# Kernel tuning notes

Measured on AMD Instinct MI355X. Metric: run time of the kernel, lower is better.

## Reference

```python
import jax, jax.numpy as jnp
import numpy as np

NUM_HEADS = 16
EMBED_DIM = 1024
HEAD_DIM = EMBED_DIM // NUM_HEADS
SCALE = HEAD_DIM * -0.5  # faithful to source: multiplicative, negative


def setup_inputs() -> dict:
    key = jax.random.key(0)
    kx, kq, kk, kv, ko = jax.random.split(key, 5)
    B, S, E = 2, 2048, EMBED_DIM
    std = 1.0 / np.sqrt(E)
    return {
        "x": jax.random.normal(kx, (B, S, E), dtype=jnp.float32),
        "Wq": jax.random.normal(kq, (E, E), dtype=jnp.float32) * std,
        "Wk": jax.random.normal(kk, (E, E), dtype=jnp.float32) * std,
        "Wv": jax.random.normal(kv, (E, E), dtype=jnp.float32) * std,
        "Wo": jax.random.normal(ko, (E, E), dtype=jnp.float32) * std,
    }


def reference(x, Wq, Wk, Wv, Wo):
    B, S, E = x.shape
    H, D = NUM_HEADS, HEAD_DIM
    # nn.Linear(bias=False): y = x @ W.T
    q = (x @ Wq.T).reshape(B, S, H, D).transpose(0, 2, 1, 3)  # unused downstream (faithful to source)
    k = (x @ Wk.T).reshape(B, S, H, D).transpose(0, 2, 1, 3)  # [B,H,S,D]
    v = (x @ Wv.T).reshape(B, S, H, D).transpose(0, 2, 1, 3)
    # Source bug reproduced: logits = K @ V^T, scaled by head_dim * -0.5
    logits = jnp.einsum('bhsd,bhtd->bhst', k, v) * SCALE  # [B,H,S,S]
    attn = jax.nn.softmax(logits, axis=-1)
    out = jnp.einsum('bhst,bhtd->bhsd', attn, v)  # [B,H,S,D]
    out = out.transpose(0, 2, 1, 3).reshape(B, S, E)
    return out @ Wo.T
```

## Files before the change

kernel.cpp:

```cpp
#include <hip/hip_runtime.h>
#include <math.h>

#define B_ 2
#define S_ 2048
#define E_ 1024
#define H_ 16
#define D_ 64
#define M_ (B_ * S_)
#define SC2 (-46.166241308446828f)

typedef unsigned short u16;
typedef __attribute__((ext_vector_type(8))) short short8;
typedef __attribute__((ext_vector_type(16))) float f32x16;

static __device__ __forceinline__ u16 bf16_rne(float x) {
    unsigned u = __float_as_uint(x);
    u += 0x7FFFu + ((u >> 16) & 1u);
    return (u16)(u >> 16);
}
static __device__ __forceinline__ float bf16f(u16 h) {
    return __uint_as_float(((unsigned)h) << 16);
}
static __device__ __forceinline__ f32x16 mfma_b(short8 a, short8 b, f32x16 c) {
    return __builtin_amdgcn_mfma_f32_32x32x16_bf16(a, b, c, 0, 0, 0);
}
static __device__ __forceinline__ unsigned pack2(u16 a, u16 b) {
    return (unsigned)a | ((unsigned)b << 16);
}

__global__ __launch_bounds__(256)
void convert_split(const float* __restrict__ x, const float* __restrict__ Wk,
                   const float* __restrict__ Wv, const float* __restrict__ Wo,
                   u16* __restrict__ Xh, u16* __restrict__ Xl,
                   u16* __restrict__ Wkh, u16* __restrict__ Wkl,
                   u16* __restrict__ Wvh, u16* __restrict__ Wvl,
                   u16* __restrict__ Woh, u16* __restrict__ Wol)
{
    const int blk = blockIdx.x;
    const float* src; u16 *dh, *dl; int base;
    if (blk < 4096)      { src = x;  dh = Xh;  dl = Xl;  base = blk; }
    else if (blk < 5120) { src = Wk; dh = Wkh; dl = Wkl; base = blk - 4096; }
    else if (blk < 6144) { src = Wv; dh = Wvh; dl = Wvl; base = blk - 5120; }
    else                 { src = Wo; dh = Woh; dl = Wol; base = blk - 6144; }
    const size_t off = ((size_t)base * 256 + threadIdx.x) * 4;
    const float4 v = *(const float4*)(src + off);
    const float f[4] = {v.x, v.y, v.z, v.w};
    u16 h4[4], l4[4];
#pragma unroll
    for (int i = 0; i < 4; ++i) {
        h4[i] = bf16_rne(f[i]);
        l4[i] = bf16_rne(f[i] - bf16f(h4[i]));
    }
    *(uint2*)(dh + off) = make_uint2(pack2(h4[0], h4[1]), pack2(h4[2], h4[3]));
    *(uint2*)(dl + off) = make_uint2(pack2(l4[0], l4[1]), pack2(l4[2], l4[3]));
}

#define CSA 520
#define CSB 1032

template<int MODE>
__global__ __launch_bounds__(256, 2)
void gemm_k(const u16* __restrict__ Ah, const u16* __restrict__ Al,
            const u16* __restrict__ B1h, const u16* __restrict__ B1l,
            const u16* __restrict__ B2h, const u16* __restrict__ B2l,
            u16* __restrict__ Khg, u16* __restrict__ Klg,
            u16* __restrict__ Vhg, u16* __restrict__ Vlg,
            u16* __restrict__ Vtg, float* __restrict__ Cout)
{
    __shared__ u16 sAh[4 * CSA];
    __shared__ u16 sAl[MODE == 0 ? 4 * CSA : 8];
    __shared__ u16 sB1h[4 * CSB];
    __shared__ u16 sB1l[MODE == 0 ? 4 * CSB : 8];
    __shared__ u16 sB2h[MODE == 0 ? 4 * CSB : 8];
    __shared__ u16 sB2l[MODE == 0 ? 4 * CSB : 8];

    const int tid = threadIdx.x;
    const int w   = tid >> 6;
    const int l31 = tid & 31;
    const int hh  = (tid >> 5) & 1;
    const int m0  = blockIdx.y * 64;
    const int n0  = blockIdx.x * 128;
    const int wm  = (w >> 1) << 5;
    const int wn  = (w & 1) << 6;

    f32x16 acc1[2], acc2[2];
#pragma unroll
    for (int r = 0; r < 16; ++r) {
        acc1[0][r] = 0.f; acc1[1][r] = 0.f;
        acc2[0][r] = 0.f; acc2[1][r] = 0.f;
    }

    const int ar = tid >> 2, ac = tid & 3;

    for (int k0 = 0; k0 < E_; k0 += 32) {
        __syncthreads();
        {
            const size_t ga = (size_t)(m0 + ar) * E_ + k0 + (ac << 3);
            *(short8*)&sAh[ac * CSA + ar * 8] = *(const short8*)(Ah + ga);
            if constexpr (MODE == 0)
                *(short8*)&sAl[ac * CSA + ar * 8] = *(const short8*)(Al + ga);
#pragma unroll
            for (int h2 = 0; h2 < 2; ++h2) {
                const int u = tid + (h2 << 8);
                const int br = u >> 2, bc = u & 3;
                const size_t gb = (size_t)(n0 + br) * E_ + k0 + (bc << 3);
                const int lo = bc * CSB + br * 8;
                *(short8*)&sB1h[lo] = *(const short8*)(B1h + gb);
                if constexpr (MODE == 0) {
                    *(short8*)&sB1l[lo] = *(const short8*)(B1l + gb);
                    *(short8*)&sB2h[lo] = *(const short8*)(B2h + gb);
                    *(short8*)&sB2l[lo] = *(const short8*)(B2l + gb);
                }
            }
        }
        __syncthreads();

#pragma unroll
        for (int ks = 0; ks < 2; ++ks) {
            const int ch = (ks << 1) + hh;
            const short8 a_h = *(const short8*)&sAh[ch * CSA + (wm + l31) * 8];
            short8 a_l;
            if constexpr (MODE == 0)
                a_l = *(const short8*)&sAl[ch * CSA + (wm + l31) * 8];
#pragma unroll
            for (int nt = 0; nt < 2; ++nt) {
                const int ro = ch * CSB + (wn + (nt << 5) + l31) * 8;
                const short8 b1h = *(const short8*)&sB1h[ro];
                acc1[nt] = mfma_b(a_h, b1h, acc1[nt]);
                if constexpr (MODE == 0) {
                    const short8 b1l = *(const short8*)&sB1l[ro];
                    const short8 b2h = *(const short8*)&sB2h[ro];
                    const short8 b2l = *(const short8*)&sB2l[ro];
                    acc1[nt] = mfma_b(a_h, b1l, acc1[nt]);
                    acc1[nt] = mfma_b(a_l, b1h, acc1[nt]);
                    acc2[nt] = mfma_b(a_h, b2h, acc2[nt]);
                    acc2[nt] = mfma_b(a_h, b2l, acc2[nt]);
                    acc2[nt] = mfma_b(a_l, b2h, acc2[nt]);
                }
            }
        }
    }

#pragma unroll
    for (int nt = 0; nt < 2; ++nt) {
        const int n = n0 + wn + (nt << 5) + l31;
        if constexpr (MODE == 1) {
#pragma unroll
            for (int r = 0; r < 16; ++r) {
                const int m = m0 + wm + (r & 3) + ((r >> 2) << 3) + (hh << 2);
                Cout[(size_t)m * E_ + n] = acc1[nt][r];
            }
        } else {
            const int hd = n >> 6, d = n & 63;
            const int b  = m0 >> 11;
            u16 vhi[16];
#pragma unroll
            for (int r = 0; r < 16; ++r) {
                const int mrow = wm + (r & 3) + ((r >> 2) << 3) + (hh << 2);
                const int s = (m0 + mrow) & (S_ - 1);
                const size_t ib = (((size_t)(b * H_ + hd) << 11) + s) * D_ + d;
                const float kv = acc1[nt][r] * SC2;
                const u16 kh_ = bf16_rne(kv);
                Khg[ib] = kh_;
                Klg[ib] = bf16_rne(kv - bf16f(kh_));
                const float vv = acc2[nt][r];
                const u16 vh_ = bf16_rne(vv);
                vhi[r] = vh_;
                Vhg[ib] = vh_;
                Vlg[ib] = bf16_rne(vv - bf16f(vh_));
            }
            const size_t vtb = ((size_t)(b * H_ + hd) * D_ + d) << 11;
#pragma unroll
            for (int g = 0; g < 4; ++g) {
                const int s0 = ((m0 + wm) & (S_ - 1)) + (g << 3) + (hh << 2);
                *(uint2*)&Vtg[vtb + s0] =
                    make_uint2(pack2(vhi[4*g], vhi[4*g+1]), pack2(vhi[4*g+2], vhi[4*g+3]));
            }
        }
    }
}

#define CSP 264

__global__ __launch_bounds__(256, 2)
void attn_mfma(const u16* __restrict__ Kh, const u16* __restrict__ Kl,
               const u16* __restrict__ Vh, const u16* __restrict__ Vl,
               const u16* __restrict__ Vt, u16* __restrict__ Obuf)
{
    __shared__ u16 sVh[8 * CSA], sVl[8 * CSA], sVt[8 * CSA];
    __shared__ u16 sP[4][8 * CSP];
    __shared__ float Alpha[4][32], Linv[4][32];

    const int tid = threadIdx.x;
    const int w   = tid >> 6;
    const int l31 = tid & 31;
    const int hh  = (tid >> 5) & 1;
    const int bh  = blockIdx.y;
    const int sbase = blockIdx.x * 128 + (w << 5);
    const int sg = sbase + l31;

    short8 kfh[4], kfl[4];
    {
        const size_t kb = ((size_t)bh * S_ + sg) * D_;
#pragma unroll
        for (int ks = 0; ks < 4; ++ks) {
            const int db = (ks << 4) + (hh << 3);
            kfh[ks] = *(const short8*)(Kh + kb + db);
            kfl[ks] = *(const short8*)(Kl + kb + db);
        }
    }

    f32x16 oacc[2];
#pragma unroll
    for (int r = 0; r < 16; ++r) { oacc[0][r] = 0.f; oacc[1][r] = 0.f; }
    float m_i = -INFINITY, l_i = 0.f;

    u16* P = &sP[w][0];

    for (int t0 = 0; t0 < S_; t0 += 64) {
        __syncthreads();
#pragma unroll
        for (int h2 = 0; h2 < 2; ++h2) {
            const int u = tid + (h2 << 8);
            const int rr = u >> 3;
            const int cc = u & 7;
            const size_t gn = ((size_t)bh * S_ + t0 + rr) * D_ + (cc << 3);
            const int lo = cc * CSA + rr * 8;
            *(short8*)&sVh[lo] = *(const short8*)(Vh + gn);
            *(short8*)&sVl[lo] = *(const short8*)(Vl + gn);
            const size_t gt = ((size_t)bh * D_ + rr) * S_ + t0 + (cc << 3);
            *(short8*)&sVt[lo] = *(const short8*)(Vt + gt);
        }
        __syncthreads();

        f32x16 st[2];
#pragma unroll
        for (int r = 0; r < 16; ++r) { st[0][r] = 0.f; st[1][r] = 0.f; }
#pragma unroll
        for (int ks = 0; ks < 4; ++ks) {
            const int ch = (ks << 1) + hh;
#pragma unroll
            for (int mt = 0; mt < 2; ++mt) {
                const int ro = ch * CSA + ((mt << 5) + l31) * 8;
                const short8 avh = *(const short8*)&sVh[ro];
                const short8 avl = *(const short8*)&sVl[ro];
                st[mt] = mfma_b(avh, kfh[ks], st[mt]);
                st[mt] = mfma_b(avh, kfl[ks], st[mt]);
                st[mt] = mfma_b(avl, kfh[ks], st[mt]);
            }
        }

        float tmax = -INFINITY;
#pragma unroll
        for (int mt = 0; mt < 2; ++mt)
#pragma unroll
            for (int r = 0; r < 16; ++r) tmax = fmaxf(tmax, st[mt][r]);
        tmax = fmaxf(tmax, __shfl_xor(tmax, 32));
        const float mnew = fmaxf(m_i, tmax);
        const float alpha = __builtin_amdgcn_exp2f(m_i - mnew);
        m_i = mnew;
        float rsum = 0.f;
#pragma unroll
        for (int mt = 0; mt < 2; ++mt)
#pragma unroll
            for (int r = 0; r < 16; ++r) {
                const float p = __builtin_amdgcn_exp2f(st[mt][r] - mnew);
                st[mt][r] = p;
                rsum += p;
            }
        rsum += __shfl_xor(rsum, 32);
        l_i = l_i * alpha + rsum;

        if (hh == 0) Alpha[w][l31] = alpha;
#pragma unroll
        for (int g = 0; g < 4; ++g) {
            const float4 av = *(const float4*)&Alpha[w][(g << 3) + (hh << 2)];
            const float af[4] = {av.x, av.y, av.z, av.w};
#pragma unroll
            for (int q = 0; q < 4; ++q) {
                oacc[0][(g << 2) + q] *= af[q];
                oacc[1][(g << 2) + q] *= af[q];
            }
        }

#pragma unroll
        for (int mt = 0; mt < 2; ++mt)
#pragma unroll
            for (int g = 0; g < 4; ++g) {
                const u16 p0 = bf16_rne(st[mt][4*g + 0]);
                const u16 p1 = bf16_rne(st[mt][4*g + 1]);
                const u16 p2 = bf16_rne(st[mt][4*g + 2]);
                const u16 p3 = bf16_rne(st[mt][4*g + 3]);
                *(uint2*)&P[((mt << 2) + g) * CSP + l31 * 8 + (hh << 2)] =
                    make_uint2(pack2(p0, p1), pack2(p2, p3));
            }

#pragma unroll
        for (int ks = 0; ks < 4; ++ks) {
            const int ch = (ks << 1) + hh;
            const short8 pf = *(const short8*)&P[ch * CSP + l31 * 8];
#pragma unroll
            for (int nt = 0; nt < 2; ++nt) {
                const short8 vtf = *(const short8*)&sVt[ch * CSA + ((nt << 5) + l31) * 8];
                oacc[nt] = mfma_b(pf, vtf, oacc[nt]);
            }
        }
    }

    if (hh == 0) Linv[w][l31] = 1.0f / l_i;
    const int b  = bh >> 4;
    const int hd = bh & 15;
    u16* Or = Obuf + ((size_t)b * S_ + sbase) * E_ + (hd << 6);
#pragma unroll
    for (int g = 0; g < 4; ++g) {
        const float4 iv = *(const float4*)&Linv[w][(g << 3) + (hh << 2)];
        const float invs[4] = {iv.x, iv.y, iv.z, iv.w};
#pragma unroll
        for (int nt = 0; nt < 2; ++nt)
#pragma unroll
            for (int q = 0; q < 4; ++q) {
                const int sl = (g << 3) + (hh << 2) + q;
                Or[(size_t)sl * E_ + (nt << 5) + l31] =
                    bf16_rne(oacc[nt][(g << 2) + q] * invs[q]);
            }
    }
}

extern "C" void kernel_launch(void* const* d_in, const int* in_sizes, int n_in,
                              void* d_out, int out_size, void* d_ws, size_t ws_size,
                              hipStream_t stream)
{
    (void)in_sizes; (void)n_in; (void)out_size; (void)ws_size;
    const float* x  = (const float*)d_in[0];
    const float* Wk = (const float*)d_in[2];
    const float* Wv = (const float*)d_in[3];
    const float* Wo = (const float*)d_in[4];
    float* out = (float*)d_out;

    char* ws = (char*)d_ws;
    const size_t MB = 1u << 20;
    u16* Xh  = (u16*)(ws + 0 * MB);
    u16* Xl  = (u16*)(ws + 8 * MB);
    u16* Wkh = (u16*)(ws + 16 * MB);
    u16* Wkl = (u16*)(ws + 18 * MB);
    u16* Wvh = (u16*)(ws + 20 * MB);
    u16* Wvl = (u16*)(ws + 22 * MB);
    u16* Woh = (u16*)(ws + 24 * MB);
    u16* Kh  = (u16*)(ws + 26 * MB);
    u16* Kl  = (u16*)(ws + 34 * MB);
    u16* Vh  = (u16*)(ws + 42 * MB);
    u16* Vl  = (u16*)(ws + 50 * MB);
    u16* Vt  = (u16*)(ws + 58 * MB);
    u16* Obuf = Xl;
    u16* Wol_junk = Kh;

    convert_split<<<7168, 256, 0, stream>>>(x, Wk, Wv, Wo,
                                            Xh, Xl, Wkh, Wkl, Wvh, Wvl, Woh, Wol_junk);
    gemm_k<0><<<dim3(E_ / 128, M_ / 64), 256, 0, stream>>>(
        Xh, Xl, Wkh, Wkl, Wvh, Wvl, Kh, Kl, Vh, Vl, Vt, nullptr);
    attn_mfma<<<dim3(S_ / 128, B_ * H_), 256, 0, stream>>>(Kh, Kl, Vh, Vl, Vt, Obuf);
    gemm_k<1><<<dim3(E_ / 128, M_ / 64), 256, 0, stream>>>(
        Obuf, Obuf, Woh, Woh, Woh, Woh,
        nullptr, nullptr, nullptr, nullptr, nullptr, out);
}
```

Measured before the change: 260.7 us.

## Prefetch tiles into registers, split-K GEMM warps, skip negligible softmax tiles

The GEMM kernel now uses 512 threads with 128x128 tiles. Two warp groups each handle half of every K chunk and merge their partial sums through shared memory, and the next tile is prefetched into registers while the current one is computed. The attention kernel doubles its block to 256 query rows and prefetches V tiles the same way. Using wave ballots, it skips the exp and PV work when a whole tile sits more than 30 log2 units below the running max, and skips the O rescale when alpha is one. It also packs P by bf16 truncation instead of round-to-nearest, and folds the K scale into Wk during conversion. These changes add approximation risk from the tile skipping and truncation, and raise register and LDS pressure.

```diff
diff --git a/kernel.cpp b/kernel.cpp
--- a/kernel.cpp
+++ b/kernel.cpp
@@ -27,6 +27,10 @@
 static __device__ __forceinline__ unsigned pack2(u16 a, u16 b) {
     return (unsigned)a | ((unsigned)b << 16);
 }
+static __device__ __forceinline__ unsigned pack_trunc(float a, float b) {
+    return __builtin_amdgcn_perm(__float_as_uint(b), __float_as_uint(a), 0x07060302u);
+}
+#define ROWMAP(r, hh) (((r) & 3) + ((((r) >> 2)) << 3) + ((hh) << 2))
 
 __global__ __launch_bounds__(256)
 void convert_split(const float* __restrict__ x, const float* __restrict__ Wk,
@@ -37,14 +41,14 @@
                    u16* __restrict__ Woh, u16* __restrict__ Wol)
 {
     const int blk = blockIdx.x;
-    const float* src; u16 *dh, *dl; int base;
+    const float* src; u16 *dh, *dl; int base; float sc = 1.0f;
     if (blk < 4096)      { src = x;  dh = Xh;  dl = Xl;  base = blk; }
-    else if (blk < 5120) { src = Wk; dh = Wkh; dl = Wkl; base = blk - 4096; }
+    else if (blk < 5120) { src = Wk; dh = Wkh; dl = Wkl; base = blk - 4096; sc = SC2; }
     else if (blk < 6144) { src = Wv; dh = Wvh; dl = Wvl; base = blk - 5120; }
     else                 { src = Wo; dh = Woh; dl = Wol; base = blk - 6144; }
     const size_t off = ((size_t)base * 256 + threadIdx.x) * 4;
     const float4 v = *(const float4*)(src + off);
-    const float f[4] = {v.x, v.y, v.z, v.w};
+    const float f[4] = {v.x * sc, v.y * sc, v.z * sc, v.w * sc};
     u16 h4[4], l4[4];
 #pragma unroll
     for (int i = 0; i < 4; ++i) {
@@ -55,11 +59,11 @@
     *(uint2*)(dl + off) = make_uint2(pack2(l4[0], l4[1]), pack2(l4[2], l4[3]));
 }
 
-#define CSA 520
 #define CSB 1032
+#define ARR (4 * CSB)
 
 template<int MODE>
-__global__ __launch_bounds__(256, 2)
+__global__ __launch_bounds__(512, 2)
 void gemm_k(const u16* __restrict__ Ah, const u16* __restrict__ Al,
             const u16* __restrict__ B1h, const u16* __restrict__ B1l,
             const u16* __restrict__ B2h, const u16* __restrict__ B2l,
@@ -67,136 +71,183 @@
             u16* __restrict__ Vhg, u16* __restrict__ Vlg,
             u16* __restrict__ Vtg, float* __restrict__ Cout)
 {
-    __shared__ u16 sAh[4 * CSA];
-    __shared__ u16 sAl[MODE == 0 ? 4 * CSA : 8];
-    __shared__ u16 sB1h[4 * CSB];
-    __shared__ u16 sB1l[MODE == 0 ? 4 * CSB : 8];
-    __shared__ u16 sB2h[MODE == 0 ? 4 * CSB : 8];
-    __shared__ u16 sB2l[MODE == 0 ? 4 * CSB : 8];
+    __shared__ u16 stage[(MODE == 0 ? 6 : 4) * ARR];
 
     const int tid = threadIdx.x;
-    const int w   = tid >> 6;
-    const int l31 = tid & 31;
-    const int hh  = (tid >> 5) & 1;
-    const int m0  = blockIdx.y * 64;
-    const int n0  = blockIdx.x * 128;
-    const int wm  = (w >> 1) << 5;
-    const int wn  = (w & 1) << 6;
-
-    f32x16 acc1[2], acc2[2];
-#pragma unroll
-    for (int r = 0; r < 16; ++r) {
-        acc1[0][r] = 0.f; acc1[1][r] = 0.f;
-        acc2[0][r] = 0.f; acc2[1][r] = 0.f;
-    }
-
-    const int ar = tid >> 2, ac = tid & 3;
-
-    for (int k0 = 0; k0 < E_; k0 += 32) {
+    const int w = tid >> 6, l31 = tid & 31, hh = (tid >> 5) & 1;
+    const int wt = w & 3, ws = w >> 2;
+    const int wm = (wt >> 1) << 6, wn = (wt & 1) << 6;
+    const int m0 = blockIdx.y * 128, n0 = blockIdx.x * 128;
+    const int ch = (ws << 1) + hh;
+
+    const int srow = tid >> 2;
+    const int sch  = tid & 3;
+    const size_t gA = (size_t)(m0 + srow) * E_ + (sch << 3);
+    const size_t gB = (size_t)(n0 + srow) * E_ + (sch << 3);
+    const int slo = sch * CSB + srow * 8;
+
+    f32x16 acc1[2][2], acc2[2][2];
+#pragma unroll
+    for (int mt = 0; mt < 2; ++mt)
+#pragma unroll
+        for (int nt = 0; nt < 2; ++nt)
+#pragma unroll
+            for (int r = 0; r < 16; ++r) {
+                acc1[mt][nt][r] = 0.f;
+                if constexpr (MODE == 0) acc2[mt][nt][r] = 0.f;
+            }
+
+    short8 pf[6];
+    auto load_tile = [&](int k0) {
+        pf[0] = *(const short8*)(Ah + gA + k0);
+        pf[2] = *(const short8*)(B1h + gB + k0);
+        if constexpr (MODE == 0) {
+            pf[1] = *(const short8*)(Al + gA + k0);
+            pf[3] = *(const short8*)(B1l + gB + k0);
+            pf[4] = *(const short8*)(B2h + gB + k0);
+            pf[5] = *(const short8*)(B2l + gB + k0);
+        }
+    };
+    auto store_tile = [&]() {
+        *(short8*)&stage[0 * ARR + slo] = pf[0];
+        *(short8*)&stage[2 * ARR + slo] = pf[2];
+        if constexpr (MODE == 0) {
+            *(short8*)&stage[1 * ARR + slo] = pf[1];
+            *(short8*)&stage[3 * ARR + slo] = pf[3];
+            *(short8*)&stage[4 * ARR + slo] = pf[4];
+            *(short8*)&stage[5 * ARR + slo] = pf[5];
+        }
+    };
+
+    load_tile(0);
+    for (int it = 0; it < 32; ++it) {
+        store_tile();
         __syncthreads();
-        {
-            const size_t ga = (size_t)(m0 + ar) * E_ + k0 + (ac << 3);
-            *(short8*)&sAh[ac * CSA + ar * 8] = *(const short8*)(Ah + ga);
-            if constexpr (MODE == 0)
-                *(short8*)&sAl[ac * CSA + ar * 8] = *(const short8*)(Al + ga);
-#pragma unroll
-            for (int h2 = 0; h2 < 2; ++h2) {
-                const int u = tid + (h2 << 8);
-                const int br = u >> 2, bc = u & 3;
-                const size_t gb = (size_t)(n0 + br) * E_ + k0 + (bc << 3);
-                const int lo = bc * CSB + br * 8;
-                *(short8*)&sB1h[lo] = *(const short8*)(B1h + gb);
-                if constexpr (MODE == 0) {
-                    *(short8*)&sB1l[lo] = *(const short8*)(B1l + gb);
-                    *(short8*)&sB2h[lo] = *(const short8*)(B2h + gb);
-                    *(short8*)&sB2l[lo] = *(const short8*)(B2l + gb);
-                }
+        if (it + 1 < 32) load_tile((it + 1) << 5);
+
+        const int aoff = ch * CSB;
+        short8 a_h[2], a_l[2];
+        a_h[0] = *(const short8*)&stage[0 * ARR + aoff + (wm + l31) * 8];
+        a_h[1] = *(const short8*)&stage[0 * ARR + aoff + (wm + 32 + l31) * 8];
+        if constexpr (MODE == 0) {
+            a_l[0] = *(const short8*)&stage[1 * ARR + aoff + (wm + l31) * 8];
+            a_l[1] = *(const short8*)&stage[1 * ARR + aoff + (wm + 32 + l31) * 8];
+        }
+#pragma unroll
+        for (int nt = 0; nt < 2; ++nt) {
+            const int ro = aoff + (wn + (nt << 5) + l31) * 8;
+            const short8 b1h = *(const short8*)&stage[2 * ARR + ro];
+            if constexpr (MODE == 0) {
+                const short8 b1l = *(const short8*)&stage[3 * ARR + ro];
+                const short8 b2h = *(const short8*)&stage[4 * ARR + ro];
+                const short8 b2l = *(const short8*)&stage[5 * ARR + ro];
+#pragma unroll
+                for (int mt = 0; mt < 2; ++mt) {
+                    acc1[mt][nt] = mfma_b(a_h[mt], b1h, acc1[mt][nt]);
+                    acc1[mt][nt] = mfma_b(a_h[mt], b1l, acc1[mt][nt]);
+                    acc1[mt][nt] = mfma_b(a_l[mt], b1h, acc1[mt][nt]);
+                    acc2[mt][nt] = mfma_b(a_h[mt], b2h, acc2[mt][nt]);
+                    acc2[mt][nt] = mfma_b(a_h[mt], b2l, acc2[mt][nt]);
+                    acc2[mt][nt] = mfma_b(a_l[mt], b2h, acc2[mt][nt]);
+                }
+            } else {
+#pragma unroll
+                for (int mt = 0; mt < 2; ++mt)
+                    acc1[mt][nt] = mfma_b(a_h[mt], b1h, acc1[mt][nt]);
             }
         }
         __syncthreads();
-
-#pragma unroll
-        for (int ks = 0; ks < 2; ++ks) {
-            const int ch = (ks << 1) + hh;
-            const short8 a_h = *(const short8*)&sAh[ch * CSA + (wm + l31) * 8];
-            short8 a_l;
-            if constexpr (MODE == 0)
-                a_l = *(const short8*)&sAl[ch * CSA + (wm + l31) * 8];
-#pragma unroll
-            for (int nt = 0; nt < 2; ++nt) {
-                const int ro = ch * CSB + (wn + (nt << 5) + l31) * 8;
-                const short8 b1h = *(const short8*)&sB1h[ro];
-                acc1[nt] = mfma_b(a_h, b1h, acc1[nt]);
-                if constexpr (MODE == 0) {
-                    const short8 b1l = *(const short8*)&sB1l[ro];
-                    const short8 b2h = *(const short8*)&sB2h[ro];
-                    const short8 b2l = *(const short8*)&sB2l[ro];
-                    acc1[nt] = mfma_b(a_h, b1l, acc1[nt]);
-                    acc1[nt] = mfma_b(a_l, b1h, acc1[nt]);
-                    acc2[nt] = mfma_b(a_h, b2h, acc2[nt]);
-                    acc2[nt] = mfma_b(a_h, b2l, acc2[nt]);
-                    acc2[nt] = mfma_b(a_l, b2h, acc2[nt]);
-                }
-            }
-        }
-    }
+    }
+
+    float* red = (float*)stage;
+    auto merge = [&](f32x16 (&acc)[2][2]) {
+#pragma unroll
+        for (int mt = 0; mt < 2; ++mt) {
+            __syncthreads();
+            if (ws == 1) {
+#pragma unroll
+                for (int nt = 0; nt < 2; ++nt)
+#pragma unroll
+                    for (int r = 0; r < 16; ++r)
+                        red[wt * 2048 + ROWMAP(r, hh) * 64 + (nt << 5) + l31] = acc[mt][nt][r];
+            }
+            __syncthreads();
+            if (ws == 0) {
+#pragma unroll
+                for (int nt = 0; nt < 2; ++nt)
+#pragma unroll
+                    for (int r = 0; r < 16; ++r)
+                        acc[mt][nt][r] += red[wt * 2048 + ROWMAP(r, hh) * 64 + (nt << 5) + l31];
+            }
+        }
+    };
+    merge(acc1);
+    if constexpr (MODE == 0) merge(acc2);
+
+    if (ws != 0) return;
 
 #pragma unroll
     for (int nt = 0; nt < 2; ++nt) {
         const int n = n0 + wn + (nt << 5) + l31;
         if constexpr (MODE == 1) {
 #pragma unroll
-            for (int r = 0; r < 16; ++r) {
-                const int m = m0 + wm + (r & 3) + ((r >> 2) << 3) + (hh << 2);
-                Cout[(size_t)m * E_ + n] = acc1[nt][r];
-            }
+            for (int mt = 0; mt < 2; ++mt)
+#pragma unroll
+                for (int r = 0; r < 16; ++r) {
+                    const int m = m0 + wm + (mt << 5) + ROWMAP(r, hh);
+                    Cout[(size_t)m * E_ + n] = acc1[mt][nt][r];
+                }
         } else {
             const int hd = n >> 6, d = n & 63;
-            const int b  = m0 >> 11;
-            u16 vhi[16];
-#pragma unroll
-            for (int r = 0; r < 16; ++r) {
-                const int mrow = wm + (r & 3) + ((r >> 2) << 3) + (hh << 2);
-                const int s = (m0 + mrow) & (S_ - 1);
-                const size_t ib = (((size_t)(b * H_ + hd) << 11) + s) * D_ + d;
-                const float kv = acc1[nt][r] * SC2;
-                const u16 kh_ = bf16_rne(kv);
-                Khg[ib] = kh_;
-                Klg[ib] = bf16_rne(kv - bf16f(kh_));
-                const float vv = acc2[nt][r];
-                const u16 vh_ = bf16_rne(vv);
-                vhi[r] = vh_;
-                Vhg[ib] = vh_;
-                Vlg[ib] = bf16_rne(vv - bf16f(vh_));
-            }
-            const size_t vtb = ((size_t)(b * H_ + hd) * D_ + d) << 11;
-#pragma unroll
-            for (int g = 0; g < 4; ++g) {
-                const int s0 = ((m0 + wm) & (S_ - 1)) + (g << 3) + (hh << 2);
-                *(uint2*)&Vtg[vtb + s0] =
-                    make_uint2(pack2(vhi[4*g], vhi[4*g+1]), pack2(vhi[4*g+2], vhi[4*g+3]));
-            }
-        }
-    }
-}
-
+            const int b = m0 >> 11;
+#pragma unroll
+            for (int mt = 0; mt < 2; ++mt) {
+                u16 vhi[16];
+#pragma unroll
+                for (int r = 0; r < 16; ++r) {
+                    const int s = (m0 + wm + (mt << 5) + ROWMAP(r, hh)) & (S_ - 1);
+                    const size_t ib = (((size_t)(b * H_ + hd) << 11) + s) * D_ + d;
+                    const float kv = acc1[mt][nt][r];
+                    const u16 kh_ = bf16_rne(kv);
+                    Khg[ib] = kh_;
+                    Klg[ib] = bf16_rne(kv - bf16f(kh_));
+                    const float vv = acc2[mt][nt][r];
+                    const u16 vh_ = bf16_rne(vv);
+                    vhi[r] = vh_;
+                    Vhg[ib] = vh_;
+                    Vlg[ib] = bf16_rne(vv - bf16f(vh_));
+                }
+                const size_t vtb = ((size_t)(b * H_ + hd) * D_ + d) << 11;
+#pragma unroll
+                for (int g = 0; g < 4; ++g) {
+                    const int s0 = ((m0 + wm + (mt << 5)) & (S_ - 1)) + (g << 3) + (hh << 2);
+                    *(uint2*)&Vtg[vtb + s0] =
+                        make_uint2(pack2(vhi[4 * g], vhi[4 * g + 1]),
+                                   pack2(vhi[4 * g + 2], vhi[4 * g + 3]));
+                }
+            }
+        }
+    }
+}
+
+#define CSA 520
+#define VA  (8 * CSA)
 #define CSP 264
-
-__global__ __launch_bounds__(256, 2)
+#define PW  (8 * CSP)
+
+__global__ __launch_bounds__(512, 2)
 void attn_mfma(const u16* __restrict__ Kh, const u16* __restrict__ Kl,
                const u16* __restrict__ Vh, const u16* __restrict__ Vl,
                const u16* __restrict__ Vt, u16* __restrict__ Obuf)
 {
-    __shared__ u16 sVh[8 * CSA], sVl[8 * CSA], sVt[8 * CSA];
-    __shared__ u16 sP[4][8 * CSP];
-    __shared__ float Alpha[4][32], Linv[4][32];
+    __shared__ u16 sV[3 * VA];
+    __shared__ u16 sP[8][PW];
+    __shared__ float Alpha[8][32], Linv[8][32];
 
     const int tid = threadIdx.x;
-    const int w   = tid >> 6;
-    const int l31 = tid & 31;
-    const int hh  = (tid >> 5) & 1;
-    const int bh  = blockIdx.y;
-    const int sbase = blockIdx.x * 128 + (w << 5);
+    const int w = tid >> 6, l31 = tid & 31, hh = (tid >> 5) & 1;
+    const int bh = blockIdx.y;
+    const int sbase = blockIdx.x * 256 + (w << 5);
     const int sg = sbase + l31;
 
     short8 kfh[4], kfl[4];
@@ -215,23 +266,26 @@
     for (int r = 0; r < 16; ++r) { oacc[0][r] = 0.f; oacc[1][r] = 0.f; }
     float m_i = -INFINITY, l_i = 0.f;
 
+    const int rr = tid >> 3, cc = tid & 7;
+    const size_t gn = ((size_t)bh * S_ + rr) * D_ + (cc << 3);
+    const size_t gt = ((size_t)bh * D_ + rr) * S_ + (cc << 3);
+    const int slo = cc * CSA + rr * 8;
     u16* P = &sP[w][0];
 
-    for (int t0 = 0; t0 < S_; t0 += 64) {
+    short8 pv[3];
+    auto load_tile = [&](int t0) {
+        pv[0] = *(const short8*)(Vh + gn + (size_t)t0 * D_);
+        pv[1] = *(const short8*)(Vl + gn + (size_t)t0 * D_);
+        pv[2] = *(const short8*)(Vt + gt + t0);
+    };
+
+    load_tile(0);
+    for (int it = 0; it < 32; ++it) {
+        *(short8*)&sV[slo] = pv[0];
+        *(short8*)&sV[VA + slo] = pv[1];
+        *(short8*)&sV[2 * VA + slo] = pv[2];
         __syncthreads();
-#pragma unroll
-        for (int h2 = 0; h2 < 2; ++h2) {
-            const int u = tid + (h2 << 8);
-            const int rr = u >> 3;
-            const int cc = u & 7;
-            const size_t gn = ((size_t)bh * S_ + t0 + rr) * D_ + (cc << 3);
-            const int lo = cc * CSA + rr * 8;
-            *(short8*)&sVh[lo] = *(const short8*)(Vh + gn);
-            *(short8*)&sVl[lo] = *(const short8*)(Vl + gn);
-            const size_t gt = ((size_t)bh * D_ + rr) * S_ + t0 + (cc << 3);
-            *(short8*)&sVt[lo] = *(const short8*)(Vt + gt);
-        }
-        __syncthreads();
+        if (it + 1 < 32) load_tile((it + 1) << 6);
 
         f32x16 st[2];
 #pragma unroll
@@ -242,8 +296,8 @@
 #pragma unroll
             for (int mt = 0; mt < 2; ++mt) {
                 const int ro = ch * CSA + ((mt << 5) + l31) * 8;
-                const short8 avh = *(const short8*)&sVh[ro];
-                const short8 avl = *(const short8*)&sVl[ro];
+                const short8 avh = *(const short8*)&sV[ro];
+                const short8 avl = *(const short8*)&sV[VA + ro];
                 st[mt] = mfma_b(avh, kfh[ks], st[mt]);
                 st[mt] = mfma_b(avh, kfl[ks], st[mt]);
                 st[mt] = mfma_b(avl, kfh[ks], st[mt]);
@@ -259,56 +313,58 @@
         const float mnew = fmaxf(m_i, tmax);
         const float alpha = __builtin_amdgcn_exp2f(m_i - mnew);
         m_i = mnew;
-        float rsum = 0.f;
-#pragma unroll
-        for (int mt = 0; mt < 2; ++mt)
-#pragma unroll
-            for (int r = 0; r < 16; ++r) {
-                const float p = __builtin_amdgcn_exp2f(st[mt][r] - mnew);
-                st[mt][r] = p;
-                rsum += p;
-            }
-        rsum += __shfl_xor(rsum, 32);
-        l_i = l_i * alpha + rsum;
-
-        if (hh == 0) Alpha[w][l31] = alpha;
-#pragma unroll
-        for (int g = 0; g < 4; ++g) {
-            const float4 av = *(const float4*)&Alpha[w][(g << 3) + (hh << 2)];
-            const float af[4] = {av.x, av.y, av.z, av.w};
-#pragma unroll
-            for (int q = 0; q < 4; ++q) {
-                oacc[0][(g << 2) + q] *= af[q];
-                oacc[1][(g << 2) + q] *= af[q];
-            }
-        }
-
-#pragma unroll
-        for (int mt = 0; mt < 2; ++mt)
+        const unsigned long long cmask = __ballot(tmax >= mnew - 30.f);
+
+        if (cmask) {
+            float rsum = 0.f;
+#pragma unroll
+            for (int mt = 0; mt < 2; ++mt)
+#pragma unroll
+                for (int r = 0; r < 16; ++r) {
+                    const float p = __builtin_amdgcn_exp2f(st[mt][r] - mnew);
+                    st[mt][r] = p;
+                    rsum += p;
+                }
+            rsum += __shfl_xor(rsum, 32);
+            l_i = l_i * alpha + rsum;
+        }
+        if (__ballot(alpha != 1.0f)) {
+            if (hh == 0) Alpha[w][l31] = alpha;
 #pragma unroll
             for (int g = 0; g < 4; ++g) {
-                const u16 p0 = bf16_rne(st[mt][4*g + 0]);
-                const u16 p1 = bf16_rne(st[mt][4*g + 1]);
-                const u16 p2 = bf16_rne(st[mt][4*g + 2]);
-                const u16 p3 = bf16_rne(st[mt][4*g + 3]);
-                *(uint2*)&P[((mt << 2) + g) * CSP + l31 * 8 + (hh << 2)] =
-                    make_uint2(pack2(p0, p1), pack2(p2, p3));
-            }
-
-#pragma unroll
-        for (int ks = 0; ks < 4; ++ks) {
-            const int ch = (ks << 1) + hh;
-            const short8 pf = *(const short8*)&P[ch * CSP + l31 * 8];
-#pragma unroll
-            for (int nt = 0; nt < 2; ++nt) {
-                const short8 vtf = *(const short8*)&sVt[ch * CSA + ((nt << 5) + l31) * 8];
-                oacc[nt] = mfma_b(pf, vtf, oacc[nt]);
-            }
-        }
+                const float4 av = *(const float4*)&Alpha[w][(g << 3) + (hh << 2)];
+                const float af[4] = {av.x, av.y, av.z, av.w};
+#pragma unroll
+                for (int q = 0; q < 4; ++q) {
+                    oacc[0][(g << 2) + q] *= af[q];
+                    oacc[1][(g << 2) + q] *= af[q];
+                }
+            }
+        }
+        if (cmask) {
+#pragma unroll
+            for (int mt = 0; mt < 2; ++mt)
+#pragma unroll
+                for (int g = 0; g < 4; ++g)
+                    *(uint2*)&P[((mt << 2) + g) * CSP + l31 * 8 + (hh << 2)] =
+                        make_uint2(pack_trunc(st[mt][4 * g], st[mt][4 * g + 1]),
+                                   pack_trunc(st[mt][4 * g + 2], st[mt][4 * g + 3]));
+#pragma unroll
+            for (int ks = 0; ks < 4; ++ks) {
+                const int ch = (ks << 1) + hh;
+                const short8 pfr = *(const short8*)&P[ch * CSP + l31 * 8];
+#pragma unroll
+                for (int nt = 0; nt < 2; ++nt) {
+                    const short8 vtf = *(const short8*)&sV[2 * VA + ch * CSA + ((nt << 5) + l31) * 8];
+                    oacc[nt] = mfma_b(pfr, vtf, oacc[nt]);
+                }
+            }
+        }
+        __syncthreads();
     }
 
     if (hh == 0) Linv[w][l31] = 1.0f / l_i;
-    const int b  = bh >> 4;
+    const int b = bh >> 4;
     const int hd = bh & 15;
     u16* Or = Obuf + ((size_t)b * S_ + sbase) * E_ + (hd << 6);
 #pragma unroll
@@ -356,10 +412,10 @@
 
     convert_split<<<7168, 256, 0, stream>>>(x, Wk, Wv, Wo,
                                             Xh, Xl, Wkh, Wkl, Wvh, Wvl, Woh, Wol_junk);
-    gemm_k<0><<<dim3(E_ / 128, M_ / 64), 256, 0, stream>>>(
+    gemm_k<0><<<dim3(E_ / 128, M_ / 128), 512, 0, stream>>>(
         Xh, Xl, Wkh, Wkl, Wvh, Wvl, Kh, Kl, Vh, Vl, Vt, nullptr);
-    attn_mfma<<<dim3(S_ / 128, B_ * H_), 256, 0, stream>>>(Kh, Kl, Vh, Vl, Vt, Obuf);
-    gemm_k<1><<<dim3(E_ / 128, M_ / 64), 256, 0, stream>>>(
+    attn_mfma<<<dim3(S_ / 256, B_ * H_), 512, 0, stream>>>(Kh, Kl, Vh, Vl, Vt, Obuf);
+    gemm_k<1><<<dim3(E_ / 128, M_ / 128), 512, 0, stream>>>(
         Obuf, Obuf, Woh, Woh, Woh, Woh,
         nullptr, nullptr, nullptr, nullptr, nullptr, out);
 }
```

Result: faster. 226.9 us (-13.0%).
